# Kernel optimization log

Hardware: AMD Instinct MI355X
Metric: run time of the kernel (lower is better)

## Reference

```python
import jax, jax.numpy as jnp
import numpy as np

B, C, N, T, R = 16, 64, 307, 288, 10  # R = low-rank dim of W1/W2

def setup_inputs() -> dict:
    key = jax.random.key(0)
    k1, k2, k3, k4 = jax.random.split(key, 4)
    x = jax.random.normal(k1, (B, C, N, T), dtype=jnp.float32)
    # Learned parameters (randomized here; module initializes them to zeros)
    W1 = jax.random.normal(k2, (R, N), dtype=jnp.float32) * 0.1
    W2 = jax.random.normal(k3, (R, N), dtype=jnp.float32) * 0.1
    alpha = jax.random.normal(k4, (C,), dtype=jnp.float32) * 0.1
    return {"x": x, "W1": W1, "W2": W2, "alpha": alpha}

def reference(x, W1, W2, alpha):
    # K = Q = einsum('bint,i->btn'): channel reduction weighted by alpha -> [B, T, N]
    K = jnp.einsum('bint,i->btn', x, alpha)
    KW1 = jnp.einsum('btn,rn->btr', K, W1)   # [B, T, R]
    QW2 = jnp.einsum('btn,rn->btr', K, W2)   # [B, T, R]
    scores = jnp.einsum('btr,bsr->bts', KW1, QW2)  # [B, T, T]
    A = jax.nn.softmax(scores, axis=-1)
    # Reweight x over the time axis: [B,T,T] x [B,C,N,T] -> [B,C,N,T]
    return jnp.einsum('bts,bcns->bcnt', A, x)
```

## Files before the change

### kernel.cpp

```cpp
#include <hip/hip_runtime.h>

#define B_ 16
#define C_ 64
#define N_ 307
#define T_ 288
#define R_ 10
#define M_ (C_ * N_)
#define TT_ (T_ / 16)
#define ST_ (T_ / 32)

typedef __attribute__((ext_vector_type(8))) short bf16x8;
typedef __attribute__((ext_vector_type(4))) float f32x4;
typedef __attribute__((ext_vector_type(4))) unsigned int u32x4;
typedef __attribute__((ext_vector_type(2))) unsigned int u32x2;

__device__ __forceinline__ unsigned short f2bf(float f) {
    unsigned int u = __float_as_uint(f);
    unsigned int r = (u + 0x7fffu + ((u >> 16) & 1u)) >> 16;
    return (unsigned short)r;
}
__device__ __forceinline__ unsigned int pack2(float a, float b) {
    return (unsigned int)f2bf(a) | ((unsigned int)f2bf(b) << 16);
}
__device__ __forceinline__ u32x4 pack8v(f32x4 a, f32x4 b) {
    u32x4 w;
    w.x = pack2(a.x, a.y); w.y = pack2(a.z, a.w);
    w.z = pack2(b.x, b.y); w.w = pack2(b.z, b.w);
    return w;
}
__device__ __forceinline__ unsigned int cvtpk2(float lo, float hi) {
    unsigned int r;
    asm("v_cvt_pk_bf16_f32 %0, %1, %2" : "=v"(r) : "v"(lo), "v"(hi));
    return r;
}

template <int WRITE_BF>
__global__ __launch_bounds__(256) void k_reduce(const float* __restrict__ x,
                                                const float* __restrict__ alpha,
                                                float* __restrict__ Kt,
                                                unsigned short* __restrict__ xbf) {
    __shared__ float a_s[C_];
    if (threadIdx.x < C_) a_s[threadIdx.x] = alpha[threadIdx.x];
    __syncthreads();
    const int T4 = T_ / 4;
    int idx = blockIdx.x * blockDim.x + threadIdx.x;
    const int total = B_ * N_ * T4;
    if (idx >= total) return;
    int t4 = idx % T4;
    int n = (idx / T4) % N_;
    int b = idx / (N_ * T4);
    const size_t chs = (size_t)N_ * T_;
    size_t base = ((size_t)(b * C_) * N_ + n) * T_ + t4 * 4;
    f32x4 s = {0.f, 0.f, 0.f, 0.f};
#pragma unroll 8
    for (int i = 0; i < C_; ++i) {
        f32x4 v = __builtin_nontemporal_load((const f32x4*)(x + base + (size_t)i * chs));
        s += a_s[i] * v;
        if (WRITE_BF) {
            u32x2 w;
            w.x = cvtpk2(v.x, v.y);
            w.y = cvtpk2(v.z, v.w);
            *(u32x2*)(xbf + base + (size_t)i * chs) = w;
        }
    }
    *(f32x4*)(Kt + ((size_t)b * N_ + n) * T_ + t4 * 4) = s;
}

#define PG 8
__global__ __launch_bounds__(256) void k_proj(const float* __restrict__ Kt,
                                              const float* __restrict__ W1,
                                              const float* __restrict__ W2,
                                              float* __restrict__ KW1,
                                              float* __restrict__ QW2) {
    __shared__ float Ws[2 * R_ * N_];
    __shared__ float part[PG][32][2 * R_];
    for (int e = threadIdx.x; e < R_ * N_; e += 256) {
        Ws[e] = W1[e];
        Ws[R_ * N_ + e] = W2[e];
    }
    __syncthreads();
    int b = blockIdx.x / (T_ / 32);
    int tc = blockIdx.x % (T_ / 32);
    int t0 = tc * 32;
    int g = threadIdx.x >> 5;
    int tl = threadIdx.x & 31;
    int n0 = g * 38 + (g < 3 ? g : 3);
    int n1 = n0 + 38 + (g < 3 ? 1 : 0);
    float a[2 * R_];
#pragma unroll
    for (int r = 0; r < 2 * R_; ++r) a[r] = 0.f;
    const float* kp = Kt + (size_t)b * N_ * T_ + t0 + tl;
    for (int n = n0; n < n1; ++n) {
        float kv = kp[(size_t)n * T_];
#pragma unroll
        for (int r = 0; r < R_; ++r) {
            a[r] += kv * Ws[r * N_ + n];
            a[R_ + r] += kv * Ws[R_ * N_ + r * N_ + n];
        }
    }
#pragma unroll
    for (int r = 0; r < 2 * R_; ++r) part[g][tl][r] = a[r];
    __syncthreads();
    for (int o = threadIdx.x; o < 32 * 2 * R_; o += 256) {
        int tl2 = o / (2 * R_);
        int rr = o % (2 * R_);
        float s = 0.f;
#pragma unroll
        for (int gg = 0; gg < PG; ++gg) s += part[gg][tl2][rr];
        int t = t0 + tl2;
        if (rr < R_) KW1[((size_t)b * T_ + t) * R_ + rr] = s;
        else         QW2[((size_t)b * T_ + t) * R_ + rr - R_] = s;
    }
}

__global__ __launch_bounds__(64) void k_softmax(const float* __restrict__ KW1,
                                                const float* __restrict__ QW2,
                                                unsigned short* __restrict__ Apk) {
    __shared__ __align__(16) unsigned short sm[T_];
    int bt = blockIdx.x;
    int b = bt / T_;
    int t = bt % T_;
    int lane = threadIdx.x;
    float kw[R_];
#pragma unroll
    for (int r = 0; r < R_; ++r) kw[r] = KW1[bt * R_ + r];
    float sc[5];
    float mx = -1e30f;
#pragma unroll
    for (int j = 0; j < 5; ++j) {
        int s = lane + j * 64;
        float v = -1e30f;
        if (s < T_) {
            const float* q = QW2 + ((size_t)b * T_ + s) * R_;
            v = 0.f;
#pragma unroll
            for (int r = 0; r < R_; ++r) v += kw[r] * q[r];
        }
        sc[j] = v;
        mx = fmaxf(mx, v);
    }
#pragma unroll
    for (int off = 32; off > 0; off >>= 1) mx = fmaxf(mx, __shfl_xor(mx, off));
    float sum = 0.f;
#pragma unroll
    for (int j = 0; j < 5; ++j) {
        int s = lane + j * 64;
        float e = (s < T_) ? __expf(sc[j] - mx) : 0.f;
        sc[j] = e;
        sum += e;
    }
#pragma unroll
    for (int off = 32; off > 0; off >>= 1) sum += __shfl_xor(sum, off);
    float inv = 1.f / sum;
#pragma unroll
    for (int j = 0; j < 5; ++j) {
        int s = lane + j * 64;
        if (s < T_) sm[s] = f2bf(sc[j] * inv);
    }
    __syncthreads();
    if (lane < 36) {
        int st = lane >> 2, q = lane & 3;
        u32x4 v = *(const u32x4*)&sm[st * 32 + q * 8];
        int tt = t >> 4, tl = t & 15;
        size_t dst = ((((size_t)b * TT_ + tt) * ST_ + st) * 64 + tl + 16 * q) * 8;
        *(u32x4*)(Apk + dst) = v;
    }
}

template <int XBF>
__global__ __launch_bounds__(256, 4) void k_out(const float* __restrict__ xf,
                                                const unsigned short* __restrict__ xb,
                                                const unsigned short* __restrict__ Apk,
                                                float* __restrict__ out) {
    const int m0 = blockIdx.x * 64;
    const int b = blockIdx.y;

    __shared__ __align__(16) unsigned short Xs[64][296];

    const int tid = threadIdx.x;
    const int lane = tid & 63;
    const int wid = tid >> 6;
    const int wm = wid & 1;
    const int wt = wid >> 1;
    const int c = lane & 15;
    const int kq = lane >> 4;

    {
        const size_t Xg = ((size_t)b * M_ + m0) * T_;
#pragma unroll
        for (int u = 0; u < 9; ++u) {
            int e = tid + u * 256;
            int row = e / 36;
            int ch = e % 36;
            if (XBF) {
                u32x4 v = __builtin_nontemporal_load((const u32x4*)(xb + Xg + (size_t)row * T_ + ch * 8));
                *(u32x4*)&Xs[row][ch * 8] = v;
            } else {
                f32x4 v0 = __builtin_nontemporal_load((const f32x4*)(xf + Xg + (size_t)row * T_ + ch * 8));
                f32x4 v1 = __builtin_nontemporal_load((const f32x4*)(xf + Xg + (size_t)row * T_ + ch * 8 + 4));
                *(u32x4*)&Xs[row][ch * 8] = pack8v(v0, v1);
            }
        }
    }
    __syncthreads();

    float* Ob = out + ((size_t)b * M_ + m0) * T_;
    const unsigned short* Abase =
        Apk + (((size_t)b * TT_ + wt * 3) * ST_) * 512 + (size_t)lane * 8;

    f32x4 acc[3][2];
    bf16x8 abuf[4][3];

#pragma unroll
    for (int d = 0; d < 4; ++d)
#pragma unroll
        for (int j = 0; j < 3; ++j)
            abuf[d][j] = *(const bf16x8*)(Abase + ((size_t)(d / 9) * 6 + j) * (ST_ * 512) + (size_t)(d % 9) * 512);

#pragma unroll
    for (int it = 0; it < 27; ++it) {
        const int k = it % 9;
        const int chunk = it / 9;
        if (k == 0) {
#pragma unroll
            for (int j = 0; j < 3; ++j)
#pragma unroll
                for (int i = 0; i < 2; ++i) acc[j][i] = (f32x4){0.f, 0.f, 0.f, 0.f};
        }
        bf16x8 tmp[3];
        if (it + 4 < 27) {
            const int nit = it + 4;
#pragma unroll
            for (int j = 0; j < 3; ++j)
                tmp[j] = *(const bf16x8*)(Abase + ((size_t)(nit / 9) * 6 + j) * (ST_ * 512) + (size_t)(nit % 9) * 512);
        }
        bf16x8 x0 = *(const bf16x8*)&Xs[wm * 32 + c][k * 32 + kq * 8];
        bf16x8 x1 = *(const bf16x8*)&Xs[wm * 32 + 16 + c][k * 32 + kq * 8];
        __builtin_amdgcn_s_setprio(1);
        acc[0][0] = __builtin_amdgcn_mfma_f32_16x16x32_bf16(abuf[it % 4][0], x0, acc[0][0], 0, 0, 0);
        acc[0][1] = __builtin_amdgcn_mfma_f32_16x16x32_bf16(abuf[it % 4][0], x1, acc[0][1], 0, 0, 0);
        acc[1][0] = __builtin_amdgcn_mfma_f32_16x16x32_bf16(abuf[it % 4][1], x0, acc[1][0], 0, 0, 0);
        acc[1][1] = __builtin_amdgcn_mfma_f32_16x16x32_bf16(abuf[it % 4][1], x1, acc[1][1], 0, 0, 0);
        acc[2][0] = __builtin_amdgcn_mfma_f32_16x16x32_bf16(abuf[it % 4][2], x0, acc[2][0], 0, 0, 0);
        acc[2][1] = __builtin_amdgcn_mfma_f32_16x16x32_bf16(abuf[it % 4][2], x1, acc[2][1], 0, 0, 0);
        __builtin_amdgcn_s_setprio(0);
        if (it + 4 < 27) {
#pragma unroll
            for (int j = 0; j < 3; ++j) abuf[it % 4][j] = tmp[j];
        }
        if (k == 8) {
            const int tb = chunk * 96 + wt * 48;
#pragma unroll
            for (int j = 0; j < 3; ++j) {
                int t = tb + j * 16 + kq * 4;
#pragma unroll
                for (int i = 0; i < 2; ++i) {
                    int m = wm * 32 + i * 16 + c;
                    __builtin_nontemporal_store(acc[j][i], (f32x4*)&Ob[(size_t)m * T_ + t]);
                }
            }
        }
    }
}

extern "C" void kernel_launch(void* const* d_in, const int* in_sizes, int n_in,
                              void* d_out, int out_size, void* d_ws, size_t ws_size,
                              hipStream_t stream) {
    const float* x = (const float*)d_in[0];
    const float* W1 = (const float*)d_in[1];
    const float* W2 = (const float*)d_in[2];
    const float* alpha = (const float*)d_in[3];
    float* out = (float*)d_out;

    char* ws = (char*)d_ws;
    float* Kt = (float*)ws;                      ws += (size_t)B_ * N_ * T_ * 4;
    float* KW1 = (float*)ws;                     ws += (size_t)B_ * T_ * R_ * 4;
    float* QW2 = (float*)ws;                     ws += (size_t)B_ * T_ * R_ * 4;
    unsigned short* Apk = (unsigned short*)ws;   ws += (size_t)B_ * TT_ * ST_ * 512 * 2;
    unsigned short* xbf = (unsigned short*)ws;
    size_t need = (size_t)(ws - (char*)d_ws) + (size_t)B_ * C_ * N_ * T_ * 2;
    const bool use_bf = (ws_size >= need);

    {
        int total = B_ * N_ * (T_ / 4);
        int blks = (total + 255) / 256;
        if (use_bf)
            k_reduce<1><<<blks, 256, 0, stream>>>(x, alpha, Kt, xbf);
        else
            k_reduce<0><<<blks, 256, 0, stream>>>(x, alpha, Kt, xbf);
    }
    k_proj<<<B_ * (T_ / 32), 256, 0, stream>>>(Kt, W1, W2, KW1, QW2);
    k_softmax<<<B_ * T_, 64, 0, stream>>>(KW1, QW2, Apk);
    {
        dim3 grid(M_ / 64, B_);
        if (use_bf)
            k_out<1><<<grid, 256, 0, stream>>>(nullptr, xbf, Apk, out);
        else
            k_out<0><<<grid, 256, 0, stream>>>(x, nullptr, Apk, out);
    }
}
```

Measured before the change: 234.3 us.

## Retile k_out to 32-row blocks with six waves each covering a T slice

Reworks the output GEMM kernel so each block handles 32 rows of the C*N dimension with 384 threads. Each of the six waves owns a 48-wide slice of output time and performs a single 9-step K loop. The earlier layout used 64 rows and 4 waves, each looping over three time chunks. This halves shared memory per block and doubles the grid, aiming for more resident blocks and better latency hiding. The cost is that each A fragment is reused across only 32 rows, so A is loaded from global/L2 twice as often per row.

Measured after the change: 224.2 us. 1.05x faster.

```diff
diff --git a/kernel.cpp b/kernel.cpp
--- a/kernel.cpp
+++ b/kernel.cpp
@@ -168,28 +168,26 @@
 }
 
 template <int XBF>
-__global__ __launch_bounds__(256, 4) void k_out(const float* __restrict__ xf,
+__global__ __launch_bounds__(384, 5) void k_out(const float* __restrict__ xf,
                                                 const unsigned short* __restrict__ xb,
                                                 const unsigned short* __restrict__ Apk,
                                                 float* __restrict__ out) {
-    const int m0 = blockIdx.x * 64;
+    const int m0 = blockIdx.x * 32;
     const int b = blockIdx.y;
 
-    __shared__ __align__(16) unsigned short Xs[64][296];
+    __shared__ __align__(16) unsigned short Xs[32][296];
 
     const int tid = threadIdx.x;
     const int lane = tid & 63;
     const int wid = tid >> 6;
-    const int wm = wid & 1;
-    const int wt = wid >> 1;
     const int c = lane & 15;
     const int kq = lane >> 4;
 
     {
         const size_t Xg = ((size_t)b * M_ + m0) * T_;
 #pragma unroll
-        for (int u = 0; u < 9; ++u) {
-            int e = tid + u * 256;
+        for (int u = 0; u < 3; ++u) {
+            int e = tid + u * 384;
             int row = e / 36;
             int ch = e % 36;
             if (XBF) {
@@ -206,59 +204,52 @@
 
     float* Ob = out + ((size_t)b * M_ + m0) * T_;
     const unsigned short* Abase =
-        Apk + (((size_t)b * TT_ + wt * 3) * ST_) * 512 + (size_t)lane * 8;
+        Apk + (((size_t)b * TT_ + wid * 3) * ST_) * 512 + (size_t)lane * 8;
 
     f32x4 acc[3][2];
-    bf16x8 abuf[4][3];
-
-#pragma unroll
-    for (int d = 0; d < 4; ++d)
+#pragma unroll
+    for (int j = 0; j < 3; ++j)
+#pragma unroll
+        for (int i = 0; i < 2; ++i) acc[j][i] = (f32x4){0.f, 0.f, 0.f, 0.f};
+
+    bf16x8 abuf[3][3];
+#pragma unroll
+    for (int d = 0; d < 3; ++d)
 #pragma unroll
         for (int j = 0; j < 3; ++j)
-            abuf[d][j] = *(const bf16x8*)(Abase + ((size_t)(d / 9) * 6 + j) * (ST_ * 512) + (size_t)(d % 9) * 512);
-
-#pragma unroll
-    for (int it = 0; it < 27; ++it) {
-        const int k = it % 9;
-        const int chunk = it / 9;
-        if (k == 0) {
+            abuf[d][j] = *(const bf16x8*)(Abase + (size_t)j * (ST_ * 512) + (size_t)d * 512);
+
+#pragma unroll
+    for (int k = 0; k < 9; ++k) {
+        bf16x8 tmp[3];
+        if (k + 3 < 9) {
 #pragma unroll
             for (int j = 0; j < 3; ++j)
-#pragma unroll
-                for (int i = 0; i < 2; ++i) acc[j][i] = (f32x4){0.f, 0.f, 0.f, 0.f};
-        }
-        bf16x8 tmp[3];
-        if (it + 4 < 27) {
-            const int nit = it + 4;
-#pragma unroll
-            for (int j = 0; j < 3; ++j)
-                tmp[j] = *(const bf16x8*)(Abase + ((size_t)(nit / 9) * 6 + j) * (ST_ * 512) + (size_t)(nit % 9) * 512);
-        }
-        bf16x8 x0 = *(const bf16x8*)&Xs[wm * 32 + c][k * 32 + kq * 8];
-        bf16x8 x1 = *(const bf16x8*)&Xs[wm * 32 + 16 + c][k * 32 + kq * 8];
+                tmp[j] = *(const bf16x8*)(Abase + (size_t)j * (ST_ * 512) + (size_t)(k + 3) * 512);
+        }
+        bf16x8 x0 = *(const bf16x8*)&Xs[c][k * 32 + kq * 8];
+        bf16x8 x1 = *(const bf16x8*)&Xs[16 + c][k * 32 + kq * 8];
         __builtin_amdgcn_s_setprio(1);
-        acc[0][0] = __builtin_amdgcn_mfma_f32_16x16x32_bf16(abuf[it % 4][0], x0, acc[0][0], 0, 0, 0);
-        acc[0][1] = __builtin_amdgcn_mfma_f32_16x16x32_bf16(abuf[it % 4][0], x1, acc[0][1], 0, 0, 0);
-        acc[1][0] = __builtin_amdgcn_mfma_f32_16x16x32_bf16(abuf[it % 4][1], x0, acc[1][0], 0, 0, 0);
-        acc[1][1] = __builtin_amdgcn_mfma_f32_16x16x32_bf16(abuf[it % 4][1], x1, acc[1][1], 0, 0, 0);
-        acc[2][0] = __builtin_amdgcn_mfma_f32_16x16x32_bf16(abuf[it % 4][2], x0, acc[2][0], 0, 0, 0);
-        acc[2][1] = __builtin_amdgcn_mfma_f32_16x16x32_bf16(abuf[it % 4][2], x1, acc[2][1], 0, 0, 0);
+        acc[0][0] = __builtin_amdgcn_mfma_f32_16x16x32_bf16(abuf[k % 3][0], x0, acc[0][0], 0, 0, 0);
+        acc[0][1] = __builtin_amdgcn_mfma_f32_16x16x32_bf16(abuf[k % 3][0], x1, acc[0][1], 0, 0, 0);
+        acc[1][0] = __builtin_amdgcn_mfma_f32_16x16x32_bf16(abuf[k % 3][1], x0, acc[1][0], 0, 0, 0);
+        acc[1][1] = __builtin_amdgcn_mfma_f32_16x16x32_bf16(abuf[k % 3][1], x1, acc[1][1], 0, 0, 0);
+        acc[2][0] = __builtin_amdgcn_mfma_f32_16x16x32_bf16(abuf[k % 3][2], x0, acc[2][0], 0, 0, 0);
+        acc[2][1] = __builtin_amdgcn_mfma_f32_16x16x32_bf16(abuf[k % 3][2], x1, acc[2][1], 0, 0, 0);
         __builtin_amdgcn_s_setprio(0);
-        if (it + 4 < 27) {
-#pragma unroll
-            for (int j = 0; j < 3; ++j) abuf[it % 4][j] = tmp[j];
-        }
-        if (k == 8) {
-            const int tb = chunk * 96 + wt * 48;
-#pragma unroll
-            for (int j = 0; j < 3; ++j) {
-                int t = tb + j * 16 + kq * 4;
-#pragma unroll
-                for (int i = 0; i < 2; ++i) {
-                    int m = wm * 32 + i * 16 + c;
-                    __builtin_nontemporal_store(acc[j][i], (f32x4*)&Ob[(size_t)m * T_ + t]);
-                }
-            }
+        if (k + 3 < 9) {
+#pragma unroll
+            for (int j = 0; j < 3; ++j) abuf[k % 3][j] = tmp[j];
+        }
+    }
+
+#pragma unroll
+    for (int j = 0; j < 3; ++j) {
+        int t = wid * 48 + j * 16 + kq * 4;
+#pragma unroll
+        for (int i = 0; i < 2; ++i) {
+            int m = i * 16 + c;
+            __builtin_nontemporal_store(acc[j][i], (f32x4*)&Ob[(size_t)m * T_ + t]);
         }
     }
 }
@@ -292,10 +283,10 @@
     k_proj<<<B_ * (T_ / 32), 256, 0, stream>>>(Kt, W1, W2, KW1, QW2);
     k_softmax<<<B_ * T_, 64, 0, stream>>>(KW1, QW2, Apk);
     {
-        dim3 grid(M_ / 64, B_);
+        dim3 grid(M_ / 32, B_);
         if (use_bf)
-            k_out<1><<<grid, 256, 0, stream>>>(nullptr, xbf, Apk, out);
+            k_out<1><<<grid, 384, 0, stream>>>(nullptr, xbf, Apk, out);
         else
-            k_out<0><<<grid, 256, 0, stream>>>(x, nullptr, Apk, out);
-    }
-}
+            k_out<0><<<grid, 384, 0, stream>>>(x, nullptr, Apk, out);
+    }
+}
```
